# Kernel tuning notes

Hardware: AMD Instinct MI355X
Metric: run time of the kernel (lower is better)

Reference implementation:

```python
import jax, jax.numpy as jnp
import numpy as np


def conv2d(x, w, pad, groups=1):
    # x: [B,Cin,H,W], w: [Cout,Cin/groups,K,K]
    return jax.lax.conv_general_dilated(
        x, w, (1, 1), [(pad, pad), (pad, pad)],
        dimension_numbers=('NCHW', 'OIHW', 'NCHW'),
        feature_group_count=groups)


def setup_inputs() -> dict:
    key = jax.random.key(0)
    ks = jax.random.split(key, 24)
    B, C, H, W = 16, 512, 32, 128          # batch, encoder_dim, feature map
    Da, Ds, De, Dm = 512, 256, 256, 1024   # att_dim, state_dim, embed_dim, mem_dim
    V, Dmerge = 1000, 512
    K, P = 11, 5
    Din = De + C + Dm                       # GRU input dim = 1792
    s = 0.02
    rn = lambda k, shp, sc=1.0: jax.random.normal(k, shp, jnp.float32) * sc
    return {
        'encode': rn(ks[0], (B, C, H, W)),
        'encode_pro': rn(ks[1], (B, Da, H, W)),
        'encode_mask': jnp.ones((B, 1, H, W), jnp.float32),
        'state': rn(ks[2], (B, Ds)),
        'pre_weight': jax.random.uniform(ks[3], (B, 1, H, W), jnp.float32),
        'cum_weight': jax.random.uniform(ks[4], (B, 1, H, W), jnp.float32),
        'context': rn(ks[5], (B, C)),
        'cond_mem': rn(ks[6], (B, Dm)),
        'cond_weight': jax.random.uniform(ks[7], (B, 2, H, W), jnp.float32),
        'label_id': jax.random.randint(ks[8], (B,), 0, V),
        # ImageAttention params (all bias-free per source)
        'w_wt': rn(ks[9], (Da, 1, K, K), s),
        'w_cwt': rn(ks[10], (Da, 1, K, K), s),
        'w_condwt': rn(ks[11], (2 * Da, 1, K, K), s),   # groups=2
        'w_energy': rn(ks[12], (Da,), s),               # 1x1 conv -> vector
        'w_state': rn(ks[13], (Da, Ds), s),
        'w_ctx': rn(ks[14], (Da, C), s),
        'w_cond': rn(ks[15], (Da, Dm), s),
        # GRU params
        'w_i2s': rn(ks[16], (Ds, Din), s), 'b_i2s': jnp.zeros((Ds,), jnp.float32),
        'w_i2g': rn(ks[17], (2 * Ds, Din), s), 'b_i2g': jnp.zeros((2 * Ds,), jnp.float32),
        'w_s2g': rn(ks[18], (2 * Ds, Ds), s),
        'w_h2h': rn(ks[19], (Ds, Ds), s),
        # Readout params
        'embed_table': rn(ks[20], (V, De), s),
        'w_l1': rn(ks[21], (Dmerge, De + Ds + C), s), 'b_l1': jnp.zeros((Dmerge,), jnp.float32),
        'w_l2': rn(ks[22], (V, Dmerge), s), 'b_l2': jnp.zeros((V,), jnp.float32),
    }


def reference(encode, encode_pro, encode_mask, state, pre_weight, cum_weight,
              context, cond_mem, cond_weight, label_id, w_wt, w_cwt, w_condwt,
              w_energy, w_state, w_ctx, w_cond, w_i2s, b_i2s, w_i2g, b_i2g,
              w_s2g, w_h2h, embed_table, w_l1, b_l1, w_l2, b_l2):
    P = (w_wt.shape[-1] - 1) // 2
    Da = w_energy.shape[0]
    B, C, H, W = encode.shape
    # --- ImageAttention ---
    t_pre = conv2d(pre_weight, w_wt, P)           # [B,Da,H,W]
    t_cum = conv2d(cum_weight, w_cwt, P)          # [B,Da,H,W]
    t_cw = conv2d(cond_weight, w_condwt, P, groups=2)
    t_cw = t_cw.reshape(B, 2, Da, H, W).sum(1)    # [B,Da,H,W]
    st = state @ w_state.T + context @ w_ctx.T + cond_mem @ w_cond.T  # [B,Da]
    concat_info = jnp.tanh(st[:, :, None, None] + t_pre + t_cum + t_cw + encode_pro)
    energies = jnp.einsum('bchw,c->bhw', concat_info, w_energy)
    energies = energies + (encode_mask[:, 0] - 1.0) * 1e8
    att = jax.nn.softmax(energies.reshape(B, H * W), axis=1)
    new_weight = att.reshape(B, 1, H, W)
    new_cum_weight = cum_weight + new_weight
    ctx = jnp.einsum('bchw,bhw->bc', encode, new_weight[:, 0])  # [B,C]
    # --- GRU transition (data = [embed, ctx, cond_mem]) ---
    embed = embed_table[label_id]
    data = jnp.concatenate([embed, ctx, cond_mem], axis=1)
    gate = data @ w_i2g.T + b_i2g + state @ w_s2g.T
    Ds = state.shape[1]
    update_g = jax.nn.sigmoid(gate[:, :Ds])
    reset_g = jax.nn.sigmoid(gate[:, Ds:])
    state_hat = jnp.tanh(data @ w_i2s.T + b_i2s + (state * reset_g) @ w_h2h.T)
    new_state = update_g * state_hat + (1.0 - update_g) * state
    # --- Readout.step ---
    merged = jnp.concatenate([embed, new_state, ctx], axis=1)
    hid = jax.nn.relu(merged @ w_l1.T + b_l1)
    readout = hid @ w_l2.T + b_l2                  # [B,V]
    return readout
```

## Files before the change

kernel.cpp:

```cpp
#include <hip/hip_runtime.h>
#include <math.h>

typedef unsigned short u16;
typedef __bf16 bf16x8 __attribute__((ext_vector_type(8)));
typedef float f32x4 __attribute__((ext_vector_type(4)));

__device__ u16   g_A_pack[16 * 512 * 32];
__device__ float g_st[16 * 512];
__device__ float g_eraw[16 * 4096];
__device__ float g_energ[16 * 4096];
__device__ float g_data[16 * 1792];
__device__ float g_merged[16 * 1024];
__device__ float g_update[16 * 256];
__device__ float g_reset[16 * 256];
__device__ float g_i2s[16 * 256];
__device__ float g_hid[16 * 512];

__device__ __forceinline__ u16 f2bf(float f) {
    unsigned u = __float_as_uint(f);
    u = (u + 0x7FFFu + ((u >> 16) & 1u)) >> 16;
    return (u16)u;
}
__device__ __forceinline__ float fast_tanh(float x) {
    return 1.0f - 2.0f / (__expf(2.0f * x) + 1.0f);
}
__device__ __forceinline__ float sigmoidf_(float x) {
    return 1.0f / (1.0f + __expf(-x));
}

__global__ void k_prep(const float* __restrict__ w_wt, const float* __restrict__ w_cwt,
                       const float* __restrict__ w_condwt) {
    int idx = blockIdx.x * blockDim.x + threadIdx.x;
    if (idx >= 512 * 512) return;
    int d = idx >> 9, k = idx & 511;
    float f = 0.f;
    if (k < 484) {
        int c = k / 121, rem = k % 121;
        if (c == 0)      f = w_wt[d * 121 + rem];
        else if (c == 1) f = w_cwt[d * 121 + rem];
        else if (c == 2) f = w_condwt[d * 121 + rem];
        else             f = w_condwt[(512 + d) * 121 + rem];
    }
    int ks = k >> 5, kl = k & 31;
    g_A_pack[(ks * 512 + d) * 32 + kl] = f2bf(f);
}

__global__ void k_st(const float* __restrict__ state, const float* __restrict__ context,
                     const float* __restrict__ cond_mem, const float* __restrict__ w_state,
                     const float* __restrict__ w_ctx, const float* __restrict__ w_cond) {
    int wid = (blockIdx.x * blockDim.x + threadIdx.x) >> 6;
    int lane = threadIdx.x & 63;
    if (wid >= 16 * 512) return;
    int b = wid >> 9, d = wid & 511;
    float acc = 0.f;
    for (int k = lane; k < 256; k += 64)  acc += state[b * 256 + k]    * w_state[d * 256 + k];
    for (int k = lane; k < 512; k += 64)  acc += context[b * 512 + k]  * w_ctx[d * 512 + k];
    for (int k = lane; k < 1024; k += 64) acc += cond_mem[b * 1024 + k] * w_cond[d * 1024 + k];
    for (int off = 32; off; off >>= 1) acc += __shfl_down(acc, off, 64);
    if (lane == 0) g_st[b * 512 + d] = acc;
}

__global__ void k_e0(const int* __restrict__ label, const float* __restrict__ embed_table,
                     const float* __restrict__ cond_mem) {
    int b = blockIdx.x, tid = threadIdx.x;
    int lbl = label[b];
    if (tid < 256) {
        float ev = embed_table[lbl * 256 + tid];
        g_data[b * 1792 + tid] = ev;
        g_merged[b * 1024 + tid] = ev;
    }
    for (int k = tid; k < 1024; k += 256)
        g_data[b * 1792 + 768 + k] = cond_mem[b * 1024 + k];
}

__global__ __launch_bounds__(512, 1) void k_conv_energy(
    const float* __restrict__ pre_w, const float* __restrict__ cum_w, const float* __restrict__ cond_w,
    const float* __restrict__ encode_pro, const float* __restrict__ w_energy)
{
    __shared__ __align__(16) u16 src[4][11][80];
    __shared__ __align__(16) u16 bchunk[2][64][40];
    __shared__ __align__(16) float epro_lds[512 * 64];
    __shared__ float ered[8][64];

    const int blk = blockIdx.x;
    const int pxh = blk & 1;
    const int h = (blk >> 1) & 31;
    const int b = blk >> 6;
    const int px0 = pxh * 64;

    const int tid = threadIdx.x;
    const int lane = tid & 63, wv = tid >> 6;
    const int lr = lane & 15, lg = lane >> 4;

    {
        const float* epbase = encode_pro + (size_t)b * 512 * 4096 + h * 128 + px0;
#pragma unroll
        for (int i = 0; i < 16; ++i) {
            int o = i * 2048 + tid * 4;
            int r = o >> 6, c = o & 63;
            float4 v = *reinterpret_cast<const float4*>(&epbase[(size_t)r * 4096 + c]);
            *reinterpret_cast<float4*>(&epro_lds[o]) = v;
        }
    }

#pragma unroll
    for (int it = 0; it < 7; ++it) {
        int t = tid + it * 512;
        if (t < 4 * 11 * 80) {
            int c = t / (11 * 80);
            int rem = t % (11 * 80);
            int i = rem / 80, x = rem % 80;
            int row = h + i - 5, w = px0 - 5 + x;
            u16 v = 0;
            if (x < 74 && row >= 0 && row < 32 && w >= 0 && w < 128) {
                const float* img = (c == 0) ? pre_w + b * 4096
                                 : (c == 1) ? cum_w + b * 4096
                                 : (c == 2) ? cond_w + b * 8192
                                            : cond_w + b * 8192 + 4096;
                v = f2bf(img[row * 128 + w]);
            }
            src[c][i][x] = v;
        }
    }
    __syncthreads();

    const int kl = tid & 31;
    const int n0 = tid >> 5;
#define BUILD(KS, BUF)                                                          \
    {                                                                           \
        int kg = (KS) * 32 + kl;                                                \
        int c = 0, i = 0, jj = 0;                                               \
        bool ok = (kg < 484);                                                   \
        if (ok) { c = kg / 121; int r2 = kg % 121; i = r2 / 11; jj = r2 % 11; } \
        _Pragma("unroll")                                                       \
        for (int rep = 0; rep < 4; ++rep) {                                     \
            int n = n0 + rep * 16;                                              \
            bchunk[BUF][n][kl] = ok ? src[c][i][n + jj] : (u16)0;               \
        }                                                                       \
    }

    f32x4 acc[4][4];
#pragma unroll
    for (int mt = 0; mt < 4; ++mt)
#pragma unroll
        for (int nt = 0; nt < 4; ++nt) {
            f32x4 z = {0.f, 0.f, 0.f, 0.f};
            acc[mt][nt] = z;
        }

    BUILD(0, 0);
    __syncthreads();

    for (int ks = 0; ks < 16; ++ks) {
        const int cur = ks & 1;
        bf16x8 afr[4];
#pragma unroll
        for (int mt = 0; mt < 4; ++mt) {
            int d = wv * 64 + mt * 16 + lr;
            afr[mt] = *reinterpret_cast<const bf16x8*>(&g_A_pack[(ks * 512 + d) * 32 + lg * 8]);
        }
        bf16x8 bfr[4];
#pragma unroll
        for (int nt = 0; nt < 4; ++nt)
            bfr[nt] = *reinterpret_cast<const bf16x8*>(&bchunk[cur][nt * 16 + lr][lg * 8]);

        if (ks < 15) BUILD(ks + 1, cur ^ 1);

#pragma unroll
        for (int mt = 0; mt < 4; ++mt)
#pragma unroll
            for (int nt = 0; nt < 4; ++nt)
                acc[mt][nt] = __builtin_amdgcn_mfma_f32_16x16x32_bf16(afr[mt], bfr[nt], acc[mt][nt], 0, 0, 0);
        __syncthreads();
    }
#undef BUILD

    float e[4] = {0.f, 0.f, 0.f, 0.f};
#pragma unroll
    for (int mt = 0; mt < 4; ++mt) {
#pragma unroll
        for (int r = 0; r < 4; ++r) {
            int d = wv * 64 + mt * 16 + lg * 4 + r;
            float stv = g_st[b * 512 + d];
            float wev = w_energy[d];
#pragma unroll
            for (int nt = 0; nt < 4; ++nt) {
                int px = nt * 16 + lr;
                float val = stv + acc[mt][nt][r] + epro_lds[d * 64 + px];
                e[nt] += wev * fast_tanh(val);
            }
        }
    }
#pragma unroll
    for (int nt = 0; nt < 4; ++nt) {
        float v = e[nt];
        v += __shfl_xor(v, 16, 64);
        v += __shfl_xor(v, 32, 64);
        if (lane < 16) ered[wv][nt * 16 + lane] = v;
    }
    __syncthreads();
    if (tid < 64) {
        float v = 0.f;
#pragma unroll
        for (int w = 0; w < 8; ++w) v += ered[w][tid];
        g_eraw[b * 4096 + h * 128 + px0 + tid] = v;
    }
}

__global__ void k_softmax(const float* __restrict__ encode_mask) {
    __shared__ float red[256];
    int b = blockIdx.x, tid = threadIdx.x;
    float v[16];
    float mx = -1e30f;
#pragma unroll
    for (int i = 0; i < 16; ++i) {
        int idx = b * 4096 + tid + i * 256;
        float ev = g_eraw[idx] + (encode_mask[idx] - 1.0f) * 1e8f;
        v[i] = ev; mx = fmaxf(mx, ev);
    }
    red[tid] = mx; __syncthreads();
    for (int s = 128; s; s >>= 1) { if (tid < s) red[tid] = fmaxf(red[tid], red[tid + s]); __syncthreads(); }
    mx = red[0]; __syncthreads();
    float sum = 0.f;
#pragma unroll
    for (int i = 0; i < 16; ++i) { v[i] = __expf(v[i] - mx); sum += v[i]; }
    red[tid] = sum; __syncthreads();
    for (int s = 128; s; s >>= 1) { if (tid < s) red[tid] += red[tid + s]; __syncthreads(); }
    float inv = 1.0f / red[0];
#pragma unroll
    for (int i = 0; i < 16; ++i) g_energ[b * 4096 + tid + i * 256] = v[i] * inv;
}

__global__ void k_ctx(const float* __restrict__ encode) {
    int wid = (blockIdx.x * blockDim.x + threadIdx.x) >> 6;
    int lane = threadIdx.x & 63;
    if (wid >= 16 * 512) return;
    int b = wid >> 9, c = wid & 511;
    const float* e = encode + (size_t)wid * 4096;
    const float* a = g_energ + b * 4096;
    float acc = 0.f;
#pragma unroll
    for (int it = 0; it < 16; ++it) {
        int base = it * 256 + lane * 4;
        float4 ev = *reinterpret_cast<const float4*>(&e[base]);
        float4 av = *reinterpret_cast<const float4*>(&a[base]);
        acc += ev.x * av.x + ev.y * av.y + ev.z * av.z + ev.w * av.w;
    }
    for (int off = 32; off; off >>= 1) acc += __shfl_down(acc, off, 64);
    if (lane == 0) { g_data[b * 1792 + 256 + c] = acc; g_merged[b * 1024 + 512 + c] = acc; }
}

__global__ void k_e1(const float* __restrict__ state,
                     const float* __restrict__ w_i2g, const float* __restrict__ b_i2g,
                     const float* __restrict__ w_s2g, const float* __restrict__ w_i2s,
                     const float* __restrict__ b_i2s) {
    int wid = (blockIdx.x * blockDim.x + threadIdx.x) >> 6;
    int lane = threadIdx.x & 63;
    if (wid >= 16 * 768) return;
    int b = wid / 768, o = wid % 768;
    const float* dt = g_data + b * 1792;
    float acc = 0.f;
    if (o < 512) {
        const float* wr = w_i2g + o * 1792;
        for (int k = lane; k < 1792; k += 64) acc += dt[k] * wr[k];
        const float* wsg = w_s2g + o * 256;
        for (int k = lane; k < 256; k += 64) acc += state[b * 256 + k] * wsg[k];
    } else {
        const float* wr = w_i2s + (o - 512) * 1792;
        for (int k = lane; k < 1792; k += 64) acc += dt[k] * wr[k];
    }
    for (int off = 32; off; off >>= 1) acc += __shfl_down(acc, off, 64);
    if (lane == 0) {
        if (o < 256)       g_update[b * 256 + o]        = sigmoidf_(acc + b_i2g[o]);
        else if (o < 512)  g_reset[b * 256 + (o - 256)] = sigmoidf_(acc + b_i2g[o]);
        else               g_i2s[b * 256 + (o - 512)]   = acc + b_i2s[o - 512];
    }
}

__global__ void k_e2(const float* __restrict__ state, const float* __restrict__ w_h2h) {
    int wid = (blockIdx.x * blockDim.x + threadIdx.x) >> 6;
    int lane = threadIdx.x & 63;
    if (wid >= 16 * 256) return;
    int b = wid >> 8, d = wid & 255;
    const float* wr = w_h2h + d * 256;
    float acc = 0.f;
    for (int k = lane; k < 256; k += 64)
        acc += state[b * 256 + k] * g_reset[b * 256 + k] * wr[k];
    for (int off = 32; off; off >>= 1) acc += __shfl_down(acc, off, 64);
    if (lane == 0) {
        float sh = fast_tanh(g_i2s[b * 256 + d] + acc);
        float u = g_update[b * 256 + d];
        g_merged[b * 1024 + 256 + d] = u * sh + (1.f - u) * state[b * 256 + d];
    }
}

__global__ void k_e3(const float* __restrict__ w_l1, const float* __restrict__ b_l1) {
    int wid = (blockIdx.x * blockDim.x + threadIdx.x) >> 6;
    int lane = threadIdx.x & 63;
    if (wid >= 16 * 512) return;
    int b = wid >> 9, m = wid & 511;
    const float* mg = g_merged + b * 1024;
    const float* wr = w_l1 + m * 1024;
    float acc = 0.f;
    for (int k = lane; k < 1024; k += 64) acc += mg[k] * wr[k];
    for (int off = 32; off; off >>= 1) acc += __shfl_down(acc, off, 64);
    if (lane == 0) g_hid[b * 512 + m] = fmaxf(acc + b_l1[m], 0.f);
}

__global__ void k_e4(const float* __restrict__ w_l2, const float* __restrict__ b_l2,
                     float* __restrict__ out) {
    int wid = (blockIdx.x * blockDim.x + threadIdx.x) >> 6;
    int lane = threadIdx.x & 63;
    if (wid >= 16 * 1000) return;
    int b = wid / 1000, v = wid % 1000;
    const float* hd = g_hid + b * 512;
    const float* wr = w_l2 + v * 512;
    float acc = 0.f;
    for (int k = lane; k < 512; k += 64) acc += hd[k] * wr[k];
    for (int off = 32; off; off >>= 1) acc += __shfl_down(acc, off, 64);
    if (lane == 0) out[b * 1000 + v] = acc + b_l2[v];
}

extern "C" void kernel_launch(void* const* d_in, const int* in_sizes, int n_in,
                              void* d_out, int out_size, void* d_ws, size_t ws_size,
                              hipStream_t stream) {
    static const int EXP[28] = {
        33554432, 33554432, 65536, 4096, 65536, 65536, 8192, 16384, 131072, 16,
        61952, 61952, 123904, 512, 131072, 262144, 524288, 458752, 256, 917504,
        512, 131072, 65536, 256000, 524288, 512, 512000, 1000};
    if (n_in != 28) return;
    for (int i = 0; i < 28; ++i)
        if (in_sizes[i] != EXP[i]) return;

    const float* encode      = (const float*)d_in[0];
    const float* encode_pro  = (const float*)d_in[1];
    const float* encode_mask = (const float*)d_in[2];
    const float* state       = (const float*)d_in[3];
    const float* pre_weight  = (const float*)d_in[4];
    const float* cum_weight  = (const float*)d_in[5];
    const float* context     = (const float*)d_in[6];
    const float* cond_mem    = (const float*)d_in[7];
    const float* cond_weight = (const float*)d_in[8];
    const int*   label_id    = (const int*)d_in[9];
    const float* w_wt     = (const float*)d_in[10];
    const float* w_cwt    = (const float*)d_in[11];
    const float* w_condwt = (const float*)d_in[12];
    const float* w_energy = (const float*)d_in[13];
    const float* w_state  = (const float*)d_in[14];
    const float* w_ctx    = (const float*)d_in[15];
    const float* w_cond   = (const float*)d_in[16];
    const float* w_i2s    = (const float*)d_in[17];
    const float* b_i2s    = (const float*)d_in[18];
    const float* w_i2g    = (const float*)d_in[19];
    const float* b_i2g    = (const float*)d_in[20];
    const float* w_s2g    = (const float*)d_in[21];
    const float* w_h2h    = (const float*)d_in[22];
    const float* embed_t  = (const float*)d_in[23];
    const float* w_l1     = (const float*)d_in[24];
    const float* b_l1     = (const float*)d_in[25];
    const float* w_l2     = (const float*)d_in[26];
    const float* b_l2     = (const float*)d_in[27];
    float* out = (float*)d_out;
    (void)d_ws; (void)ws_size;

    k_prep<<<1024, 256, 0, stream>>>(w_wt, w_cwt, w_condwt);
    k_st<<<2048, 256, 0, stream>>>(state, context, cond_mem, w_state, w_ctx, w_cond);
    k_e0<<<16, 256, 0, stream>>>(label_id, embed_t, cond_mem);
    k_conv_energy<<<1024, 512, 0, stream>>>(pre_weight, cum_weight, cond_weight,
                                            encode_pro, w_energy);
    k_softmax<<<16, 256, 0, stream>>>(encode_mask);
    k_ctx<<<2048, 256, 0, stream>>>(encode);
    k_e1<<<3072, 256, 0, stream>>>(state, w_i2g, b_i2g, w_s2g, w_i2s, b_i2s);
    k_e2<<<1024, 256, 0, stream>>>(state, w_h2h);
    k_e3<<<2048, 256, 0, stream>>>(w_l1, b_l1);
    k_e4<<<4000, 256, 0, stream>>>(w_l2, b_l2, out);
}
```

Before: 194.3 us.

## Shrink LDS in conv-energy kernel to raise occupancy via bf16 encode_pro staging

```diff
diff --git a/kernel.cpp b/kernel.cpp
--- a/kernel.cpp
+++ b/kernel.cpp
@@ -20,6 +20,9 @@
     unsigned u = __float_as_uint(f);
     u = (u + 0x7FFFu + ((u >> 16) & 1u)) >> 16;
     return (u16)u;
+}
+__device__ __forceinline__ float bf2f(u16 u) {
+    return __uint_as_float(((unsigned)u) << 16);
 }
 __device__ __forceinline__ float fast_tanh(float x) {
     return 1.0f - 2.0f / (__expf(2.0f * x) + 1.0f);
@@ -73,14 +76,13 @@
         g_data[b * 1792 + 768 + k] = cond_mem[b * 1024 + k];
 }
 
-__global__ __launch_bounds__(512, 1) void k_conv_energy(
+__global__ __launch_bounds__(512, 4) void k_conv_energy(
     const float* __restrict__ pre_w, const float* __restrict__ cum_w, const float* __restrict__ cond_w,
     const float* __restrict__ encode_pro, const float* __restrict__ w_energy)
 {
-    __shared__ __align__(16) u16 src[4][11][80];
-    __shared__ __align__(16) u16 bchunk[2][64][40];
-    __shared__ __align__(16) float epro_lds[512 * 64];
-    __shared__ float ered[8][64];
+    __shared__ __align__(16) u16 src[4][11][76];
+    __shared__ __align__(16) u16 bchunk[64][40];
+    __shared__ __align__(16) u16 epro_l[512 * 68];
 
     const int blk = blockIdx.x;
     const int pxh = blk & 1;
@@ -99,17 +101,19 @@
             int o = i * 2048 + tid * 4;
             int r = o >> 6, c = o & 63;
             float4 v = *reinterpret_cast<const float4*>(&epbase[(size_t)r * 4096 + c]);
-            *reinterpret_cast<float4*>(&epro_lds[o]) = v;
+            ushort4 s;
+            s.x = f2bf(v.x); s.y = f2bf(v.y); s.z = f2bf(v.z); s.w = f2bf(v.w);
+            *reinterpret_cast<ushort4*>(&epro_l[r * 68 + c]) = s;
         }
     }
 
 #pragma unroll
     for (int it = 0; it < 7; ++it) {
         int t = tid + it * 512;
-        if (t < 4 * 11 * 80) {
-            int c = t / (11 * 80);
-            int rem = t % (11 * 80);
-            int i = rem / 80, x = rem % 80;
+        if (t < 4 * 11 * 76) {
+            int c = t / (11 * 76);
+            int rem = t % (11 * 76);
+            int i = rem / 76, x = rem % 76;
             int row = h + i - 5, w = px0 - 5 + x;
             u16 v = 0;
             if (x < 74 && row >= 0 && row < 32 && w >= 0 && w < 128) {
@@ -126,7 +130,7 @@
 
     const int kl = tid & 31;
     const int n0 = tid >> 5;
-#define BUILD(KS, BUF)                                                          \
+#define BUILD(KS)                                                               \
     {                                                                           \
         int kg = (KS) * 32 + kl;                                                \
         int c = 0, i = 0, jj = 0;                                               \
@@ -135,7 +139,7 @@
         _Pragma("unroll")                                                       \
         for (int rep = 0; rep < 4; ++rep) {                                     \
             int n = n0 + rep * 16;                                              \
-            bchunk[BUF][n][kl] = ok ? src[c][i][n + jj] : (u16)0;               \
+            bchunk[n][kl] = ok ? src[c][i][n + jj] : (u16)0;                    \
         }                                                                       \
     }
 
@@ -148,11 +152,10 @@
             acc[mt][nt] = z;
         }
 
-    BUILD(0, 0);
+    BUILD(0);
     __syncthreads();
 
     for (int ks = 0; ks < 16; ++ks) {
-        const int cur = ks & 1;
         bf16x8 afr[4];
 #pragma unroll
         for (int mt = 0; mt < 4; ++mt) {
@@ -162,9 +165,7 @@
         bf16x8 bfr[4];
 #pragma unroll
         for (int nt = 0; nt < 4; ++nt)
-            bfr[nt] = *reinterpret_cast<const bf16x8*>(&bchunk[cur][nt * 16 + lr][lg * 8]);
-
-        if (ks < 15) BUILD(ks + 1, cur ^ 1);
+            bfr[nt] = *reinterpret_cast<const bf16x8*>(&bchunk[nt * 16 + lr][lg * 8]);
 
 #pragma unroll
         for (int mt = 0; mt < 4; ++mt)
@@ -172,6 +173,10 @@
             for (int nt = 0; nt < 4; ++nt)
                 acc[mt][nt] = __builtin_amdgcn_mfma_f32_16x16x32_bf16(afr[mt], bfr[nt], acc[mt][nt], 0, 0, 0);
         __syncthreads();
+        if (ks < 15) {
+            BUILD(ks + 1);
+            __syncthreads();
+        }
     }
 #undef BUILD
 
@@ -186,23 +191,26 @@
 #pragma unroll
             for (int nt = 0; nt < 4; ++nt) {
                 int px = nt * 16 + lr;
-                float val = stv + acc[mt][nt][r] + epro_lds[d * 64 + px];
+                float val = stv + acc[mt][nt][r] + bf2f(epro_l[d * 68 + px]);
                 e[nt] += wev * fast_tanh(val);
             }
         }
     }
+
+    float* ered = reinterpret_cast<float*>(&bchunk[0][0]);
+    __syncthreads();
 #pragma unroll
     for (int nt = 0; nt < 4; ++nt) {
         float v = e[nt];
         v += __shfl_xor(v, 16, 64);
         v += __shfl_xor(v, 32, 64);
-        if (lane < 16) ered[wv][nt * 16 + lane] = v;
+        if (lane < 16) ered[wv * 64 + nt * 16 + lane] = v;
     }
     __syncthreads();
     if (tid < 64) {
         float v = 0.f;
 #pragma unroll
-        for (int w = 0; w < 8; ++w) v += ered[w][tid];
+        for (int w = 0; w < 8; ++w) v += ered[w * 64 + tid];
         g_eraw[b * 4096 + h * 128 + px0 + tid] = v;
     }
 }
```

Result: faster. 168.4 us (-13.3%).
